# Kernel tuning notes

Measured on AMD Instinct MI355X. Metric: run time of the kernel, lower is better.

Reference implementation:

```python
import jax, jax.numpy as jnp
import numpy as np
from jax import lax

N_QUBITS = 4
DIM = 2 ** N_QUBITS  # 16, amplitude-embedding feature size == clayer_in output
N_QLAYERS = 1
INPUT_SIZE = 128
HIDDEN_SIZE = 128
BATCH = 128
SEQ = 1024


def _cnot_perm(n):
    # Composed permutation matrix of the ansatz CNOT ladder:
    # for i in 1..2: for j in range(n): CNOT(wire j -> wire (j+i) % n)
    # PennyLane wire ordering: wire 0 is the most significant bit.
    dim = 2 ** n
    gates = []
    for i in range(1, 3):
        for j in range(n):
            gates.append((j, (j + i) % n))
    P = np.eye(dim, dtype=np.float32)
    for (c, t) in gates:
        cbit, tbit = n - 1 - c, n - 1 - t
        g = np.zeros((dim, dim), dtype=np.float32)
        for s in range(dim):
            s2 = s ^ (1 << tbit) if (s >> cbit) & 1 else s
            g[s2, s] = 1.0
        P = g @ P  # psi_new = P @ psi
    return P

_P = jnp.asarray(_cnot_perm(N_QUBITS))
# Z[s, w] = <s| PauliZ(wire w) |s>
_Z = jnp.asarray(np.array([[1.0 - 2.0 * ((s >> (N_QUBITS - 1 - w)) & 1)
                            for w in range(N_QUBITS)] for s in range(DIM)],
                           dtype=np.float32))


def _rx_kron(theta):
    # kron of per-wire RX(theta_i) gates, wire 0 most significant
    c = jnp.cos(theta / 2).astype(jnp.complex64)
    s = (-1j * jnp.sin(theta / 2)).astype(jnp.complex64)
    u = None
    for i in range(N_QUBITS):
        m = jnp.stack([jnp.stack([c[i], s[i]]), jnp.stack([s[i], c[i]])])
        u = m if u is None else jnp.kron(u, m)
    return u  # (DIM, DIM) complex64


def _vqc(y, weights):
    # AmplitudeEmbedding(normalize=True) + n_qlayers x (CNOT ladder, RX layer)
    # then expval(PauliZ) on each wire. y: (B, DIM) real, weights: (L, V, n)
    norm = jnp.sqrt(jnp.sum(y * y, axis=1, keepdims=True))
    psi = (y / norm).astype(jnp.complex64)  # (B, DIM)
    for l in range(N_QLAYERS):
        psi = psi @ _P.T               # CNOT ladder (permutation)
        psi = psi @ _rx_kron(weights[l, 0]).T  # RX layer (only vrotation 0 used)
    probs = (psi * jnp.conj(psi)).real
    return probs @ _Z  # (B, n_qubits)


def _cell(h, x_t, w_r, w_r1, w_u, W_in, b_in, W_out, b_out):
    y = jnp.concatenate([h, x_t], axis=1) @ W_in + b_in
    r = jax.nn.sigmoid(_vqc(y, w_r) @ W_out + b_out)
    v1 = jnp.concatenate([r * h, x_t], axis=1) @ W_in + b_in
    h2 = jnp.tanh(_vqc(v1, w_r1) @ W_out + b_out)
    z = jax.nn.sigmoid(_vqc(y, w_u) @ W_out + b_out)
    return (1.0 - z) * h + z * h2


def _run(xs, w_r, w_r1, w_u, W_in, b_in, W_out, b_out):
    # xs: (T, B, F); returns hidden states in loop order, shape (B, T, H)
    h0 = jnp.zeros((xs.shape[1], HIDDEN_SIZE), dtype=xs.dtype)
    def step(h, x_t):
        hn = _cell(h, x_t, w_r, w_r1, w_u, W_in, b_in, W_out, b_out)
        return hn, hn
    _, hs = lax.scan(step, h0, xs)
    return jnp.swapaxes(hs, 0, 1)


def setup_inputs() -> dict:
    key = jax.random.key(0)
    ks = jax.random.split(key, 11)
    concat = INPUT_SIZE + HIDDEN_SIZE
    two_pi = 2.0 * float(np.pi)
    return {
        "x": jax.random.normal(ks[0], (BATCH, SEQ, INPUT_SIZE), jnp.float32),
        "W_in": jax.random.normal(ks[1], (concat, DIM), jnp.float32) / np.float32(np.sqrt(concat)),
        "b_in": jax.random.normal(ks[2], (DIM,), jnp.float32) * 0.01,
        "W_out": jax.random.normal(ks[3], (N_QUBITS, HIDDEN_SIZE), jnp.float32) / np.float32(np.sqrt(N_QUBITS)),
        "b_out": jax.random.normal(ks[4], (HIDDEN_SIZE,), jnp.float32) * 0.01,
        "w_reset": jax.random.uniform(ks[5], (N_QLAYERS, 1, N_QUBITS), jnp.float32, 0.0, two_pi),
        "w_reset1": jax.random.uniform(ks[6], (N_QLAYERS, 1, N_QUBITS), jnp.float32, 0.0, two_pi),
        "w_update": jax.random.uniform(ks[7], (N_QLAYERS, 1, N_QUBITS), jnp.float32, 0.0, two_pi),
        "w_back_reset": jax.random.uniform(ks[8], (N_QLAYERS, 1, N_QUBITS), jnp.float32, 0.0, two_pi),
        "w_back_reset1": jax.random.uniform(ks[9], (N_QLAYERS, 1, N_QUBITS), jnp.float32, 0.0, two_pi),
        "w_back_update": jax.random.uniform(ks[10], (N_QLAYERS, 1, N_QUBITS), jnp.float32, 0.0, two_pi),
    }


def reference(x, W_in, b_in, W_out, b_out, w_reset, w_reset1, w_update,
              w_back_reset, w_back_reset1, w_back_update):
    xs = jnp.swapaxes(x, 0, 1)  # (T, B, F)
    fwd = _run(xs, w_reset, w_reset1, w_update, W_in, b_in, W_out, b_out)
    # Original backward loop iterates t = T-1..0 and stacks in loop order,
    # then adds WITHOUT flipping back. Reproduce that exactly.
    bwd = _run(xs[::-1], w_back_reset, w_back_reset1, w_back_update,
               W_in, b_in, W_out, b_out)
    return (fwd + bwd) / 2.0
```

## Files before the change

kernel.cpp:

```cpp
#include <hip/hip_runtime.h>
#include <hip/hip_bf16.h>

#define TSEQ 1024
#define NB   128
#define HID  128
#define QDIM 16

typedef unsigned int  u32;
typedef unsigned short u16;
typedef float f32x2 __attribute__((ext_vector_type(2)));


template<int CTRL>
__device__ __forceinline__ int dpp_i(int x) {
  return __builtin_amdgcn_update_dpp(0, x, CTRL, 0xF, 0xF, true);
}
template<int CTRL>
__device__ __forceinline__ float dpp_f(float x) {
  return __int_as_float(dpp_i<CTRL>(__float_as_int(x)));
}

#ifdef __has_builtin
#if __has_builtin(__builtin_amdgcn_permlane16_swap) && __has_builtin(__builtin_amdgcn_permlane32_swap)
#define HAS_PLS 1
#endif
#endif
#ifndef HAS_PLS
#define HAS_PLS 0
#endif

__device__ __forceinline__ float pls16_sum(float x) {
#if HAS_PLS
  auto r = __builtin_amdgcn_permlane16_swap(__float_as_uint(x), __float_as_uint(x), false, false);
  return __uint_as_float(r[0]) + __uint_as_float(r[1]);
#else
  return x + __shfl_xor(x, 16, 64);
#endif
}
__device__ __forceinline__ float pls32_sum(float x) {
#if HAS_PLS
  auto r = __builtin_amdgcn_permlane32_swap(__float_as_uint(x), __float_as_uint(x), false, false);
  return __uint_as_float(r[0]) + __uint_as_float(r[1]);
#else
  return x + __shfl_xor(x, 32, 64);
#endif
}

__device__ __forceinline__ float rcpf(float x) { return __builtin_amdgcn_rcpf(x); }

__device__ __forceinline__ float ex2(float x) {
#if defined(__has_builtin)
#if __has_builtin(__builtin_amdgcn_exp2f)
  return __builtin_amdgcn_exp2f(x);
#else
  return exp2f(x);
#endif
#else
  return exp2f(x);
#endif
}

__device__ __forceinline__ u16 f2bf(float f) {
  u32 u = __float_as_uint(f);
  u32 r = (u + 0x7FFFu + ((u >> 16) & 1u)) >> 16;
  return (u16)r;
}

__device__ __forceinline__ f32x2 s2(float x) { f32x2 r; r.x = x; r.y = x; return r; }

__device__ __forceinline__ int gperm(int t) {
  int u = t;
#define APPLY(c, tt) u ^= (((u >> (3 - (c))) & 1) << (3 - (tt)));
  APPLY(3, 1) APPLY(2, 0) APPLY(1, 3) APPLY(0, 2)
  APPLY(3, 0) APPLY(2, 3) APPLY(1, 2) APPLY(0, 1)
#undef APPLY
  return u;
}


__global__ __launch_bounds__(256) void xw_kernel(
    const float* __restrict__ x, const float* __restrict__ W_in,
    const float* __restrict__ b_in, float* __restrict__ xw) {
  __shared__ __align__(16) float xs[16][132];
  __shared__ float wl[2048];
  __shared__ float bl[16];
  const int tid = threadIdx.x;
  const long r0 = (long)blockIdx.x * 16;
#pragma unroll
  for (int i = 0; i < 8; ++i) {
    int idx = tid + i * 256;
    xs[idx >> 7][idx & 127] = x[(r0 + (idx >> 7)) * 128 + (idx & 127)];
  }
#pragma unroll
  for (int i = 0; i < 8; ++i) {
    int idx = tid + i * 256;
    wl[idx] = W_in[2048 + idx];
  }
  if (tid < 16) bl[tid] = b_in[tid];
  __syncthreads();
  const int rr = tid >> 4, j = tid & 15;
  const int gj = gperm(j);
  float s = bl[gj];
#pragma unroll
  for (int k4 = 0; k4 < 32; ++k4) {
    float4 v = *reinterpret_cast<const float4*>(&xs[rr][k4 * 4]);
    int kb = k4 * 4;
    s = fmaf(v.x, wl[(kb + 0) * 16 + gj], s);
    s = fmaf(v.y, wl[(kb + 1) * 16 + gj], s);
    s = fmaf(v.z, wl[(kb + 2) * 16 + gj], s);
    s = fmaf(v.w, wl[(kb + 3) * 16 + gj], s);
  }
  xw[(r0 + rr) * 16 + j] = s;
}


template<bool BF16WS>
__global__ __launch_bounds__(64)
__attribute__((amdgpu_waves_per_eu(1, 2)))
void qbigru_main(
    const float* __restrict__ W_in,
    const float* __restrict__ W_out,
    const float* __restrict__ b_out,
    const float* __restrict__ thr_f, const float* __restrict__ thr1_f, const float* __restrict__ thu_f,
    const float* __restrict__ thr_b, const float* __restrict__ thr1_b, const float* __restrict__ thu_b,
    const float* __restrict__ xw,
    float* __restrict__ out,
    void* __restrict__ bwdws) {
  const int tid = threadIdx.x;
  const int l4  = tid & 15;
  const int dir = blockIdx.x >> 7;
  const int b   = blockIdx.x & 127;

  const int pshl = dpp_i<0x104>(tid);
  const int sel4 = (pshl == (tid ^ 4)) ? ~0 : 0;
  auto xor4f = [&](float x) {
    int a = dpp_i<0x104>(__float_as_int(x));
    int c = dpp_i<0x114>(__float_as_int(x));
    return __int_as_float((a & sel4) | (c & ~sel4));
  };

  auto bfr = [&](const float* v) -> float {
    float w1[8];
#pragma unroll
    for (int j = 0; j < 8; ++j) w1[j] = v[2 * j] + dpp_f<0xB1>(v[2 * j + 1]);
    float w2[4];
#pragma unroll
    for (int j = 0; j < 4; ++j) w2[j] = w1[2 * j] + dpp_f<0x4E>(w1[2 * j + 1]);
    float w3[2];
#pragma unroll
    for (int j = 0; j < 2; ++j) w3[j] = w2[j] + dpp_f<0x128>(w2[j + 2]);
    float y0 = w3[0] + xor4f(w3[1]);
    return pls32_sum(pls16_sum(y0));
  };

  auto ebf = [&](float p, float& n2, float* eb) {
    float s4 = xor4f(p);
    float P  = p + s4, M2 = p - s4;
    float dP = dpp_f<0x128>(P), dM2 = dpp_f<0x128>(M2);
    float P3 = P + dP, M3 = P - dP; M2 = M2 + dM2;
    float a1 = dpp_f<0x4E>(P3), a2 = dpp_f<0x4E>(M3), a3 = dpp_f<0x4E>(M2);
    float P1 = P3 + a1, M1 = P3 - a1; M3 += a2; M2 += a3;
    float b0_ = dpp_f<0xB1>(P1), b1_ = dpp_f<0xB1>(M1), b3_ = dpp_f<0xB1>(M3), b2_ = dpp_f<0xB1>(M2);
    n2 = P1 + b0_;
    eb[0] = P1 - b0_; eb[1] = M1 + b1_; eb[3] = M3 + b3_; eb[2] = M2 + b2_;
  };

  const float* thr  = dir ? thr_b  : thr_f;
  const float* thr1 = dir ? thr1_b : thr1_f;
  const float* thu  = dir ? thu_b  : thu_f;

  f32x2 w0p[8], w1p[8];
#pragma unroll
  for (int i = 0; i < 8; ++i) {
    int ja = gperm((2 * i) ^ l4), jb = gperm((2 * i + 1) ^ l4);
    f32x2 a, c;
    a.x = W_in[tid * QDIM + ja];        a.y = W_in[tid * QDIM + jb];
    c.x = W_in[(tid + 64) * QDIM + ja]; c.y = W_in[(tid + 64) * QDIM + jb];
    w0p[i] = a; w1p[i] = c;
  }

  f32x2 woRpk[4], woZpk[4], woHpk[4];
#pragma unroll
  for (int B = 0; B < 4; ++B) {
    float sgn = ((tid >> B) & 1) ? -1.f : 1.f;
    float cR = cosf(thr[3 - B])  * sgn;
    float cZ = cosf(thu[3 - B])  * sgn;
    float cH = cosf(thr1[3 - B]) * sgn;
    float wo  = W_out[(3 - B) * HID + tid];
    float wo1 = W_out[(3 - B) * HID + tid + 64];
    f32x2 rr_, zz_, hh_;
    rr_.x = wo * cR;  rr_.y = wo1 * cR;
    zz_.x = wo * cZ;  zz_.y = wo1 * cZ;
    hh_.x = wo * cH;  hh_.y = wo1 * cH;
    woRpk[B] = rr_; woZpk[B] = zz_; woHpk[B] = hh_;
  }
  const float L2E = 1.4426950408889634f;
  f32x2 nbcpk, bc2pk;
  nbcpk.x = -b_out[tid] * L2E;        nbcpk.y = -b_out[tid + 64] * L2E;
  bc2pk.x =  b_out[tid] * (2.f * L2E); bc2pk.y =  b_out[tid + 64] * (2.f * L2E);

  auto dot4pk = [](const float* e, const f32x2* w) -> f32x2 {
    f32x2 d = s2(e[0]) * w[0];
    d = s2(e[1]) * w[1] + d;
    d = s2(e[2]) * w[2] + d;
    d = s2(e[3]) * w[3] + d;
    return d;
  };

  f32x2 hpk; hpk.x = 0.f; hpk.y = 0.f;
  const float* pxw = xw + ((long)b * TSEQ + (dir ? TSEQ - 1 : 0)) * QDIM;
  const long xstep = dir ? -QDIM : QDIM;
  float xc = pxw[l4]; pxw += xstep;
  float xn = pxw[l4]; pxw += xstep;

  float* po  = out + (long)b * TSEQ * HID + tid;
  float* pbf = (float*)bwdws + (long)b * TSEQ * HID + tid;
  u16*   pbh = (u16*)bwdws + (long)b * TSEQ * HID + tid;

#pragma unroll 1
  for (int t = 0; t < TSEQ; ++t) {
    float xnn = pxw[l4]; pxw += xstep;

    f32x2 hh0 = s2(hpk.x);
    f32x2 hh1 = s2(hpk.y);
    float v[16];
#pragma unroll
    for (int i = 0; i < 8; ++i) {
      f32x2 a = hh0 * w0p[i] + hh1 * w1p[i];
      v[2 * i] = a.x; v[2 * i + 1] = a.y;
    }
    float yv = bfr(v) + xc;

    float prb = yv * yv;

    float n2, eb[4];
    ebf(prb, n2, eb);
    float inv = rcpf(n2);
    float nic = inv * (-L2E);

    f32x2 rd = dot4pk(eb, woRpk);
    f32x2 zd = dot4pk(eb, woZpk);

    f32x2 ra = rd * s2(nic) + nbcpk;
    f32x2 za = zd * s2(nic) + nbcpk;
    float r0 = rcpf(1.f + ex2(ra.x));
    float r1 = rcpf(1.f + ex2(ra.y));
    float z0 = rcpf(1.f + ex2(za.x));
    float z1 = rcpf(1.f + ex2(za.y));

    f32x2 rpk; rpk.x = r0; rpk.y = r1;
    f32x2 rh = rpk * hpk;
    hh0 = s2(rh.x);
    hh1 = s2(rh.y);
#pragma unroll
    for (int i = 0; i < 8; ++i) {
      f32x2 a = hh0 * w0p[i] + hh1 * w1p[i];
      v[2 * i] = a.x; v[2 * i + 1] = a.y;
    }
    float vv = bfr(v) + xc;

    float prb2 = vv * vv;

    float n2b, eb2[4];
    ebf(prb2, n2b, eb2);
    float invb = rcpf(n2b);
    f32x2 hd = dot4pk(eb2, woHpk);
    f32x2 ha = hd * s2(invb * (2.f * L2E)) + bc2pk;
    float h20 = fmaf(-2.f, rcpf(1.f + ex2(ha.x)), 1.f);
    float h21 = fmaf(-2.f, rcpf(1.f + ex2(ha.y)), 1.f);

    f32x2 h2pk; h2pk.x = h20; h2pk.y = h21;
    f32x2 zpk;  zpk.x  = z0;  zpk.y  = z1;
    hpk = zpk * (h2pk - hpk) + hpk;

    f32x2 opk = hpk * s2(0.5f);
    if (dir == 0) {
      po[0]  = opk.x;
      po[64] = opk.y;
      po += HID;
    } else if (BF16WS) {
      pbh[0]  = f2bf(opk.x);
      pbh[64] = f2bf(opk.y);
      pbh += HID;
    } else {
      pbf[0]  = opk.x;
      pbf[64] = opk.y;
      pbf += HID;
    }

    xc = xn; xn = xnn;
  }
}


template<bool BF16WS>
__global__ __launch_bounds__(256) void combine_k(float* __restrict__ out,
                                                 const void* __restrict__ bwd, long n4) {
  long i = (long)blockIdx.x * 256 + threadIdx.x;
  const long stride = (long)gridDim.x * 256;
  for (; i < n4; i += stride) {
    float4 o = reinterpret_cast<float4*>(out)[i];
    float ax, ay, az, aw;
    if (BF16WS) {
      ushort4 u = reinterpret_cast<const ushort4*>(bwd)[i];
      ax = __uint_as_float((u32)u.x << 16);
      ay = __uint_as_float((u32)u.y << 16);
      az = __uint_as_float((u32)u.z << 16);
      aw = __uint_as_float((u32)u.w << 16);
    } else {
      float4 a = reinterpret_cast<const float4*>(bwd)[i];
      ax = a.x; ay = a.y; az = a.z; aw = a.w;
    }
    o.x += ax; o.y += ay; o.z += az; o.w += aw;
    reinterpret_cast<float4*>(out)[i] = o;
  }
}


extern "C" void kernel_launch(void* const* d_in, const int* in_sizes, int n_in,
                              void* d_out, int out_size, void* d_ws, size_t ws_size,
                              hipStream_t stream) {
  const float* x     = (const float*)d_in[0];
  const float* W_in  = (const float*)d_in[1];
  const float* b_in  = (const float*)d_in[2];
  const float* W_out = (const float*)d_in[3];
  const float* b_out = (const float*)d_in[4];
  const float* thr_f  = (const float*)d_in[5];
  const float* thr1_f = (const float*)d_in[6];
  const float* thu_f  = (const float*)d_in[7];
  const float* thr_b  = (const float*)d_in[8];
  const float* thr1_b = (const float*)d_in[9];
  const float* thu_b  = (const float*)d_in[10];
  float* out = (float*)d_out;

  char* ws = (char*)d_ws;
  const size_t PAD = 4096;
  const size_t xw_bytes = (size_t)NB * TSEQ * QDIM * sizeof(float);
  float* xw = (float*)(ws + PAD);
  void* bwd = (void*)(ws + PAD + xw_bytes + PAD);
  const size_t need_f32 = 2 * PAD + xw_bytes + (size_t)NB * TSEQ * HID * sizeof(float);
  const bool f32ws = (ws_size >= need_f32);

  xw_kernel<<<(NB * TSEQ) / 16, 256, 0, stream>>>(x, W_in, b_in, xw);

  if (f32ws) {
    qbigru_main<false><<<256, 64, 0, stream>>>(W_in, W_out, b_out,
        thr_f, thr1_f, thu_f, thr_b, thr1_b, thu_b, xw, out, bwd);
  } else {
    qbigru_main<true><<<256, 64, 0, stream>>>(W_in, W_out, b_out,
        thr_f, thr1_f, thu_f, thr_b, thr1_b, thu_b, xw, out, bwd);
  }

  const long n4 = (long)NB * TSEQ * HID / 4;
  if (f32ws) combine_k<false><<<2048, 256, 0, stream>>>(out, bwd, n4);
  else       combine_k<true><<<2048, 256, 0, stream>>>(out, bwd, n4);
}
```

Before: 584.2 us.

## Fold log2e scaling into weights, rebalance dot4, and pair hidden units per lane

```diff
diff --git a/kernel.cpp b/kernel.cpp
--- a/kernel.cpp
+++ b/kernel.cpp
@@ -169,42 +169,42 @@
   const float* thr1 = dir ? thr1_b : thr1_f;
   const float* thu  = dir ? thu_b  : thu_f;
 
+  const int k0 = 2 * tid, k1 = 2 * tid + 1;
+
   f32x2 w0p[8], w1p[8];
 #pragma unroll
   for (int i = 0; i < 8; ++i) {
     int ja = gperm((2 * i) ^ l4), jb = gperm((2 * i + 1) ^ l4);
     f32x2 a, c;
-    a.x = W_in[tid * QDIM + ja];        a.y = W_in[tid * QDIM + jb];
-    c.x = W_in[(tid + 64) * QDIM + ja]; c.y = W_in[(tid + 64) * QDIM + jb];
+    a.x = W_in[k0 * QDIM + ja];  a.y = W_in[k0 * QDIM + jb];
+    c.x = W_in[k1 * QDIM + ja];  c.y = W_in[k1 * QDIM + jb];
     w0p[i] = a; w1p[i] = c;
   }
 
+  const float L2E = 1.4426950408889634f;
   f32x2 woRpk[4], woZpk[4], woHpk[4];
 #pragma unroll
   for (int B = 0; B < 4; ++B) {
     float sgn = ((tid >> B) & 1) ? -1.f : 1.f;
-    float cR = cosf(thr[3 - B])  * sgn;
-    float cZ = cosf(thu[3 - B])  * sgn;
-    float cH = cosf(thr1[3 - B]) * sgn;
-    float wo  = W_out[(3 - B) * HID + tid];
-    float wo1 = W_out[(3 - B) * HID + tid + 64];
+    float cR = cosf(thr[3 - B])  * sgn * (-L2E);
+    float cZ = cosf(thu[3 - B])  * sgn * (-L2E);
+    float cH = cosf(thr1[3 - B]) * sgn * (2.f * L2E);
+    float wo0 = W_out[(3 - B) * HID + k0];
+    float wo1 = W_out[(3 - B) * HID + k1];
     f32x2 rr_, zz_, hh_;
-    rr_.x = wo * cR;  rr_.y = wo1 * cR;
-    zz_.x = wo * cZ;  zz_.y = wo1 * cZ;
-    hh_.x = wo * cH;  hh_.y = wo1 * cH;
+    rr_.x = wo0 * cR;  rr_.y = wo1 * cR;
+    zz_.x = wo0 * cZ;  zz_.y = wo1 * cZ;
+    hh_.x = wo0 * cH;  hh_.y = wo1 * cH;
     woRpk[B] = rr_; woZpk[B] = zz_; woHpk[B] = hh_;
   }
-  const float L2E = 1.4426950408889634f;
   f32x2 nbcpk, bc2pk;
-  nbcpk.x = -b_out[tid] * L2E;        nbcpk.y = -b_out[tid + 64] * L2E;
-  bc2pk.x =  b_out[tid] * (2.f * L2E); bc2pk.y =  b_out[tid + 64] * (2.f * L2E);
+  nbcpk.x = -b_out[k0] * L2E;         nbcpk.y = -b_out[k1] * L2E;
+  bc2pk.x =  b_out[k0] * (2.f * L2E); bc2pk.y =  b_out[k1] * (2.f * L2E);
 
   auto dot4pk = [](const float* e, const f32x2* w) -> f32x2 {
-    f32x2 d = s2(e[0]) * w[0];
-    d = s2(e[1]) * w[1] + d;
-    d = s2(e[2]) * w[2] + d;
-    d = s2(e[3]) * w[3] + d;
-    return d;
+    f32x2 d01 = s2(e[1]) * w[1] + s2(e[0]) * w[0];
+    f32x2 d23 = s2(e[3]) * w[3] + s2(e[2]) * w[2];
+    return d01 + d23;
   };
 
   f32x2 hpk; hpk.x = 0.f; hpk.y = 0.f;
@@ -213,9 +213,9 @@
   float xc = pxw[l4]; pxw += xstep;
   float xn = pxw[l4]; pxw += xstep;
 
-  float* po  = out + (long)b * TSEQ * HID + tid;
-  float* pbf = (float*)bwdws + (long)b * TSEQ * HID + tid;
-  u16*   pbh = (u16*)bwdws + (long)b * TSEQ * HID + tid;
+  float* po  = out + (long)b * TSEQ * HID + k0;
+  float* pbf = (float*)bwdws + (long)b * TSEQ * HID + k0;
+  u32*   pbh = (u32*)bwdws + ((long)b * TSEQ * HID >> 1) + tid;
 
 #pragma unroll 1
   for (int t = 0; t < TSEQ; ++t) {
@@ -236,17 +236,21 @@
     float n2, eb[4];
     ebf(prb, n2, eb);
     float inv = rcpf(n2);
-    float nic = inv * (-L2E);
 
     f32x2 rd = dot4pk(eb, woRpk);
     f32x2 zd = dot4pk(eb, woZpk);
 
-    f32x2 ra = rd * s2(nic) + nbcpk;
-    f32x2 za = zd * s2(nic) + nbcpk;
+    f32x2 ra = rd * s2(inv) + nbcpk;
+    f32x2 za = zd * s2(inv) + nbcpk;
     float r0 = rcpf(1.f + ex2(ra.x));
     float r1 = rcpf(1.f + ex2(ra.y));
     float z0 = rcpf(1.f + ex2(za.x));
     float z1 = rcpf(1.f + ex2(za.y));
+
+    f32x2 zpk;  zpk.x = z0; zpk.y = z1;
+    f32x2 omz = s2(1.f) - zpk;
+    f32x2 qpk = omz * hpk + zpk;
+    f32x2 spk = s2(-2.f) * zpk;
 
     f32x2 rpk; rpk.x = r0; rpk.y = r1;
     f32x2 rh = rpk * hpk;
@@ -265,26 +269,21 @@
     ebf(prb2, n2b, eb2);
     float invb = rcpf(n2b);
     f32x2 hd = dot4pk(eb2, woHpk);
-    f32x2 ha = hd * s2(invb * (2.f * L2E)) + bc2pk;
-    float h20 = fmaf(-2.f, rcpf(1.f + ex2(ha.x)), 1.f);
-    float h21 = fmaf(-2.f, rcpf(1.f + ex2(ha.y)), 1.f);
-
-    f32x2 h2pk; h2pk.x = h20; h2pk.y = h21;
-    f32x2 zpk;  zpk.x  = z0;  zpk.y  = z1;
-    hpk = zpk * (h2pk - hpk) + hpk;
+    f32x2 ha = hd * s2(invb) + bc2pk;
+    float wq0 = rcpf(1.f + ex2(ha.x));
+    float wq1 = rcpf(1.f + ex2(ha.y));
+    f32x2 wpk; wpk.x = wq0; wpk.y = wq1;
+    hpk = spk * wpk + qpk;
 
     f32x2 opk = hpk * s2(0.5f);
     if (dir == 0) {
-      po[0]  = opk.x;
-      po[64] = opk.y;
+      *reinterpret_cast<f32x2*>(po) = opk;
       po += HID;
     } else if (BF16WS) {
-      pbh[0]  = f2bf(opk.x);
-      pbh[64] = f2bf(opk.y);
-      pbh += HID;
+      *pbh = (u32)f2bf(opk.x) | ((u32)f2bf(opk.y) << 16);
+      pbh += HID / 2;
     } else {
-      pbf[0]  = opk.x;
-      pbf[64] = opk.y;
+      *reinterpret_cast<f32x2*>(pbf) = opk;
       pbf += HID;
     }
 
```

Measured after the change: 590.8 us. Within noise of the previous version (+1.1%).
